# Optimization experiments

Measured on AMD Instinct MI355X. Metric: run time of the kernel, lower is better.

## Reference

```python
import jax, jax.numpy as jnp
import numpy as np

N_NODES = 50000
N_EDGES = 800000
NODE_IN = 256
EDGE_IN = 64
HEADS = 4
OUT = 64
NEG_SLOPE = 0.2  # dgl GATConv default


def setup_inputs() -> dict:
    key = jax.random.key(0)
    ks = jax.random.split(key, 10)
    node_feats = jax.random.normal(ks[0], (N_NODES, NODE_IN), dtype=jnp.float32)
    edge_feats = jax.random.normal(ks[1], (N_EDGES, EDGE_IN), dtype=jnp.float32)
    src = jax.random.randint(ks[2], (N_EDGES,), 0, N_NODES, dtype=jnp.int32)
    dst = jax.random.randint(ks[3], (N_EDGES,), 0, N_NODES, dtype=jnp.int32)
    # learned params (Xavier-ish scaling)
    W = jax.random.normal(ks[4], (NODE_IN, HEADS * OUT), dtype=jnp.float32) / np.sqrt(NODE_IN)
    We = jax.random.normal(ks[5], (EDGE_IN, HEADS * OUT), dtype=jnp.float32) / np.sqrt(EDGE_IN)
    attn_l = jax.random.normal(ks[6], (HEADS, OUT), dtype=jnp.float32) / np.sqrt(OUT)
    attn_r = jax.random.normal(ks[7], (HEADS, OUT), dtype=jnp.float32) / np.sqrt(OUT)
    attn_e = jax.random.normal(ks[8], (HEADS, OUT), dtype=jnp.float32) / np.sqrt(OUT)
    return {"node_feats": node_feats, "edge_feats": edge_feats, "W": W, "We": We,
            "attn_l": attn_l, "attn_r": attn_r, "attn_e": attn_e, "src": src, "dst": dst}


def reference(node_feats, edge_feats, W, We, attn_l, attn_r, attn_e, src, dst):
    # GAT with edge features (dropout disabled for deterministic reference).
    N = node_feats.shape[0]
    H, D = attn_l.shape
    h = (node_feats @ W).reshape(N, H, D)              # [N,H,D] projected nodes
    fe = (edge_feats @ We).reshape(-1, H, D)           # [E,H,D] projected edges
    el = jnp.sum(h * attn_l, axis=-1)                  # [N,H]
    er = jnp.sum(h * attn_r, axis=-1)                  # [N,H]
    ee = jnp.sum(fe * attn_e, axis=-1)                 # [E,H]
    e = jax.nn.leaky_relu(el[src] + er[dst] + ee, NEG_SLOPE)  # [E,H]
    # numerically stable segment softmax over incoming edges of each dst node
    emax = jax.ops.segment_max(e, dst, num_segments=N)         # [N,H]
    emax = jnp.where(jnp.isfinite(emax), emax, 0.0)            # empty segments -> 0
    ex = jnp.exp(e - emax[dst])                                # [E,H]
    denom = jax.ops.segment_sum(ex, dst, num_segments=N)       # [N,H]
    alpha = ex / (denom[dst] + 1e-9)                           # [E,H]
    out = jax.ops.segment_sum(alpha[..., None] * h[src], dst, num_segments=N)  # [N,H,D]
    return out
```

## Files before the change

### kernel.cpp

```cpp
#include <hip/hip_runtime.h>
#include <hip/hip_bf16.h>
#include <math.h>

#define N_NODES 50000
#define N_EDGES 800000
#define HEADS 4
#define HD 256
#define NEG_SLOPE 0.2f

typedef __attribute__((ext_vector_type(8))) short bf16x8;
typedef __attribute__((ext_vector_type(4))) float f32x4;

__device__ unsigned short g_Hb[N_NODES * HD];
__device__ float    g_el[N_NODES * HEADS];
__device__ float    g_er[N_NODES * HEADS];
__device__ float    g_ebuf[N_EDGES * HEADS];
__device__ float    g_esort[N_EDGES * HEADS];
__device__ int      g_srcs[N_EDGES];
__device__ int      g_deg[N_NODES];
__device__ int      g_rowptr[N_NODES + 1];
__device__ int      g_cursor[N_NODES];
__device__ int      g_bsum[256];
__device__ float    g_Wea[64 * HEADS];
__device__ unsigned short g_Wbt[256 * 256];
__device__ unsigned short g_Wlrb[16 * 256];

__device__ __forceinline__ unsigned short f2bf(float f) {
    unsigned u = __float_as_uint(f);
    u += 0x7fffu + ((u >> 16) & 1u);
    return (unsigned short)(u >> 16);
}
__device__ __forceinline__ float bf_lo(unsigned u) {
    return __uint_as_float(u << 16);
}
__device__ __forceinline__ float bf_hi(unsigned u) {
    return __uint_as_float(u & 0xFFFF0000u);
}

__global__ void k_prep2(const float* __restrict__ W, const float* __restrict__ We,
                        const float* __restrict__ al, const float* __restrict__ ar,
                        const float* __restrict__ ae) {
    int t = blockIdx.x * 256 + threadIdx.x;
    if (t < N_NODES) g_deg[t] = 0;
    if (t < 256) {
        int k = t >> 2, h = t & 3;
        float s = 0.f;
        for (int d = 0; d < 64; ++d) s += We[k * 256 + h * 64 + d] * ae[h * 64 + d];
        g_Wea[t] = s;
    }
    if (t < 4096) {
        int c = t >> 8, k = t & 255;
        float s = 0.f;
        if (c < 4) {
            for (int d = 0; d < 64; ++d) s += W[k * 256 + c * 64 + d] * al[c * 64 + d];
        } else if (c < 8) {
            int h = c - 4;
            for (int d = 0; d < 64; ++d) s += W[k * 256 + h * 64 + d] * ar[h * 64 + d];
        }
        g_Wlrb[c * 256 + k] = f2bf(s);
    }
    for (int i = t; i < 65536; i += 50176) {
        int n = i >> 8, k = i & 255;
        g_Wbt[n * 256 + k] = f2bf(W[k * 256 + n]);
    }
}

#define BM 128
#define BK 32
__global__ __launch_bounds__(256) void k_gemm_mfma(const float* __restrict__ X) {
    __shared__ unsigned short As[BM][40];
    const int tid = threadIdx.x;
    const int wave = tid >> 6, lane = tid & 63;
    const int l15 = lane & 15, lg = lane >> 4;
    const int row0 = blockIdx.x * BM;

    f32x4 acc[8][4];
    f32x4 accE[8];
    #pragma unroll
    for (int i = 0; i < 8; ++i) {
        accE[i] = (f32x4){0.f, 0.f, 0.f, 0.f};
        #pragma unroll
        for (int j = 0; j < 4; ++j) acc[i][j] = (f32x4){0.f, 0.f, 0.f, 0.f};
    }

    for (int k0 = 0; k0 < 256; k0 += BK) {
        #pragma unroll
        for (int q = 0; q < 4; ++q) {
            int f = q * 256 + tid;
            int r = f >> 3;
            int kq = (f & 7) << 2;
            int grow = row0 + r;
            float4 v = make_float4(0.f, 0.f, 0.f, 0.f);
            if (grow < N_NODES) v = *(const float4*)(X + grow * 256 + k0 + kq);
            ushort4 b;
            b.x = f2bf(v.x); b.y = f2bf(v.y); b.z = f2bf(v.z); b.w = f2bf(v.w);
            *(ushort4*)&As[r][kq] = b;
        }
        bf16x8 bfr[4];
        #pragma unroll
        for (int nf = 0; nf < 4; ++nf) {
            int n = wave * 64 + nf * 16 + l15;
            bfr[nf] = *(const bf16x8*)(g_Wbt + n * 256 + k0 + lg * 8);
        }
        bf16x8 bfrE = *(const bf16x8*)(g_Wlrb + l15 * 256 + k0 + lg * 8);
        __syncthreads();
        #pragma unroll
        for (int mf = 0; mf < 8; ++mf) {
            bf16x8 afr = *(const bf16x8*)&As[mf * 16 + l15][lg * 8];
            #pragma unroll
            for (int nf = 0; nf < 4; ++nf)
                acc[mf][nf] = __builtin_amdgcn_mfma_f32_16x16x32_bf16(
                    afr, bfr[nf], acc[mf][nf], 0, 0, 0);
            accE[mf] = __builtin_amdgcn_mfma_f32_16x16x32_bf16(
                afr, bfrE, accE[mf], 0, 0, 0);
        }
        __syncthreads();
    }
    #pragma unroll
    for (int mf = 0; mf < 8; ++mf) {
        #pragma unroll
        for (int r = 0; r < 4; ++r) {
            int grow = row0 + mf * 16 + lg * 4 + r;
            if (grow < N_NODES) {
                #pragma unroll
                for (int nf = 0; nf < 4; ++nf) {
                    int col = wave * 64 + nf * 16 + l15;
                    g_Hb[grow * 256 + col] = f2bf(acc[mf][nf][r]);
                }
                if (wave == 0) {
                    if (l15 < 4) g_el[grow * 4 + l15] = accE[mf][r];
                    else if (l15 < 8) g_er[grow * 4 + (l15 - 4)] = accE[mf][r];
                }
            }
        }
    }
}

__global__ __launch_bounds__(256) void k_edge(const float* __restrict__ EF,
                                              const int* __restrict__ src,
                                              const int* __restrict__ dst) {
    __shared__ float sEF[32][258];
    __shared__ float4 sW[64];
    const int tid = threadIdx.x;
    if (tid < 64) sW[tid] = *(const float4*)(g_Wea + tid * 4);
    const int e0 = blockIdx.x * 256;

    float p0 = 0.f, p1 = 0.f, p2 = 0.f, p3 = 0.f;
    #pragma unroll
    for (int kc = 0; kc < 2; ++kc) {
        __syncthreads();
        #pragma unroll
        for (int q = 0; q < 8; ++q) {
            int f = q * 256 + tid;
            int e = f >> 3;
            int c = (f & 7) << 2;
            float4 v = *(const float4*)(EF + (size_t)(e0 + e) * 64 + kc * 32 + c);
            sEF[c + 0][e] = v.x; sEF[c + 1][e] = v.y;
            sEF[c + 2][e] = v.z; sEF[c + 3][e] = v.w;
        }
        __syncthreads();
        #pragma unroll
        for (int k = 0; k < 32; ++k) {
            float x = sEF[k][tid];
            float4 w = sW[kc * 32 + k];
            p0 += x * w.x; p1 += x * w.y; p2 += x * w.z; p3 += x * w.w;
        }
    }
    const int eid = e0 + tid;
    const int s = src[eid], d = dst[eid];
    float4 l4 = *(const float4*)(g_el + s * 4);
    float4 r4 = *(const float4*)(g_er + d * 4);
    float e0v = p0 + l4.x + r4.x;
    float e1v = p1 + l4.y + r4.y;
    float e2v = p2 + l4.z + r4.z;
    float e3v = p3 + l4.w + r4.w;
    e0v = e0v > 0.f ? e0v : NEG_SLOPE * e0v;
    e1v = e1v > 0.f ? e1v : NEG_SLOPE * e1v;
    e2v = e2v > 0.f ? e2v : NEG_SLOPE * e2v;
    e3v = e3v > 0.f ? e3v : NEG_SLOPE * e3v;
    *(float4*)(g_ebuf + eid * 4) =
        make_float4(__expf(e0v), __expf(e1v), __expf(e2v), __expf(e3v));
    atomicAdd(&g_deg[d], 1);
}

__global__ void k_scan1() {
    __shared__ int s[256];
    int tid = threadIdx.x;
    int g = blockIdx.x * 256 + tid;
    int v = (g < N_NODES) ? g_deg[g] : 0;
    s[tid] = v; __syncthreads();
    for (int o = 1; o < 256; o <<= 1) {
        int t = (tid >= o) ? s[tid - o] : 0;
        __syncthreads();
        s[tid] += t;
        __syncthreads();
    }
    if (g < N_NODES) g_rowptr[g] = s[tid] - v;
    if (tid == 255) g_bsum[blockIdx.x] = s[255];
}

__global__ void k_scan2(int nb) {
    __shared__ int s[256];
    int tid = threadIdx.x;
    int v = (tid < nb) ? g_bsum[tid] : 0;
    s[tid] = v; __syncthreads();
    for (int o = 1; o < 256; o <<= 1) {
        int t = (tid >= o) ? s[tid - o] : 0;
        __syncthreads();
        s[tid] += t;
        __syncthreads();
    }
    if (tid < nb) g_bsum[tid] = s[tid] - v;
}

__global__ void k_scan3() {
    int g = blockIdx.x * 256 + threadIdx.x;
    if (g < N_NODES) {
        int r = g_rowptr[g] + g_bsum[blockIdx.x];
        g_rowptr[g] = r;
        g_cursor[g] = r;
    }
    if (g == 0) g_rowptr[N_NODES] = N_EDGES;
}

__global__ void k_scatter(const int* __restrict__ src, const int* __restrict__ dst) {
    int e = blockIdx.x * 256 + threadIdx.x;
    if (e < N_EDGES) {
        int p = atomicAdd(&g_cursor[dst[e]], 1);
        g_srcs[p] = src[e];
        *(float4*)(g_esort + p * 4) = *(const float4*)(g_ebuf + e * 4);
    }
}

__global__ __launch_bounds__(256) void k_agg(float* __restrict__ out) {
    int node = (blockIdx.x * 256 + threadIdx.x) >> 6;
    int lane = threadIdx.x & 63;
    if (node >= N_NODES) return;
    int start = g_rowptr[node], end = g_rowptr[node + 1];
    int myh = lane >> 4, sub = lane & 15;
    const int hoff = myh * 64 + sub * 4;

    float den = 0.f;
    float a0 = 0.f, a1 = 0.f, a2 = 0.f, a3 = 0.f;
    #pragma unroll 4
    for (int i = start; i < end; ++i) {
        float ex = g_esort[i * 4 + myh];
        int s = g_srcs[i];
        uint2 hv = *(const uint2*)(g_Hb + s * 256 + hoff);
        den += ex;
        a0 += ex * bf_lo(hv.x); a1 += ex * bf_hi(hv.x);
        a2 += ex * bf_lo(hv.y); a3 += ex * bf_hi(hv.y);
    }
    float rden = 1.0f / (den + 1e-9f);
    *(float4*)(out + node * 256 + lane * 4) =
        make_float4(a0 * rden, a1 * rden, a2 * rden, a3 * rden);
}

extern "C" void kernel_launch(void* const* d_in, const int* in_sizes, int n_in,
                              void* d_out, int out_size, void* d_ws, size_t ws_size,
                              hipStream_t stream) {
    const float* X  = (const float*)d_in[0];
    const float* EF = (const float*)d_in[1];
    const float* W  = (const float*)d_in[2];
    const float* We = (const float*)d_in[3];
    const float* al = (const float*)d_in[4];
    const float* ar = (const float*)d_in[5];
    const float* ae = (const float*)d_in[6];
    const int* src  = (const int*)d_in[7];
    const int* dst  = (const int*)d_in[8];
    float* out = (float*)d_out;

    const int nb_scan = (N_NODES + 255) / 256;

    k_prep2<<<nb_scan, 256, 0, stream>>>(W, We, al, ar, ae);
    k_gemm_mfma<<<(N_NODES + BM - 1) / BM, 256, 0, stream>>>(X);
    k_edge<<<N_EDGES / 256, 256, 0, stream>>>(EF, src, dst);
    k_scan1<<<nb_scan, 256, 0, stream>>>();
    k_scan2<<<1, 256, 0, stream>>>(nb_scan);
    k_scan3<<<nb_scan, 256, 0, stream>>>();
    k_scatter<<<(N_EDGES + 255) / 256, 256, 0, stream>>>(src, dst);
    k_agg<<<(N_NODES + 3) / 4, 256, 0, stream>>>(out);
}
```

Measured before the change: 265.6 us.

## Compute degrees upfront, scatter edge scores directly in edge kernel, single-block scan

Degree counting moves into the prep kernel, and the three-kernel scan becomes one 1024-thread block scan, so the CSR row pointers are ready before the edge kernel runs. The edge kernel then writes exp scores and source ids straight to their sorted CSR positions. This removes the separate scatter kernel and the intermediate ebuf round trip. Global buffers move to the workspace, deg is zeroed with a memset, and the aggregation unroll goes from 4 to 8. The single-block scan is serial, so it may add latency, and the atomic-ordered scatter writes from the edge kernel are uncoalesced.

```diff
diff --git a/kernel.cpp b/kernel.cpp
--- a/kernel.cpp
+++ b/kernel.cpp
@@ -11,20 +11,6 @@
 typedef __attribute__((ext_vector_type(8))) short bf16x8;
 typedef __attribute__((ext_vector_type(4))) float f32x4;
 
-__device__ unsigned short g_Hb[N_NODES * HD];
-__device__ float    g_el[N_NODES * HEADS];
-__device__ float    g_er[N_NODES * HEADS];
-__device__ float    g_ebuf[N_EDGES * HEADS];
-__device__ float    g_esort[N_EDGES * HEADS];
-__device__ int      g_srcs[N_EDGES];
-__device__ int      g_deg[N_NODES];
-__device__ int      g_rowptr[N_NODES + 1];
-__device__ int      g_cursor[N_NODES];
-__device__ int      g_bsum[256];
-__device__ float    g_Wea[64 * HEADS];
-__device__ unsigned short g_Wbt[256 * 256];
-__device__ unsigned short g_Wlrb[16 * 256];
-
 __device__ __forceinline__ unsigned short f2bf(float f) {
     unsigned u = __float_as_uint(f);
     u += 0x7fffu + ((u >> 16) & 1u);
@@ -37,16 +23,18 @@
     return __uint_as_float(u & 0xFFFF0000u);
 }
 
-__global__ void k_prep2(const float* __restrict__ W, const float* __restrict__ We,
-                        const float* __restrict__ al, const float* __restrict__ ar,
-                        const float* __restrict__ ae) {
+__global__ void k_prep(const float* __restrict__ W, const float* __restrict__ We,
+                       const float* __restrict__ al, const float* __restrict__ ar,
+                       const float* __restrict__ ae, const int* __restrict__ dst,
+                       int* __restrict__ deg, float* __restrict__ Wea,
+                       unsigned short* __restrict__ Wbt,
+                       unsigned short* __restrict__ Wlrb) {
     int t = blockIdx.x * 256 + threadIdx.x;
-    if (t < N_NODES) g_deg[t] = 0;
     if (t < 256) {
         int k = t >> 2, h = t & 3;
         float s = 0.f;
         for (int d = 0; d < 64; ++d) s += We[k * 256 + h * 64 + d] * ae[h * 64 + d];
-        g_Wea[t] = s;
+        Wea[t] = s;
     }
     if (t < 4096) {
         int c = t >> 8, k = t & 255;
@@ -57,17 +45,61 @@
             int h = c - 4;
             for (int d = 0; d < 64; ++d) s += W[k * 256 + h * 64 + d] * ar[h * 64 + d];
         }
-        g_Wlrb[c * 256 + k] = f2bf(s);
+        Wlrb[c * 256 + k] = f2bf(s);
     }
     for (int i = t; i < 65536; i += 50176) {
         int n = i >> 8, k = i & 255;
-        g_Wbt[n * 256 + k] = f2bf(W[k * 256 + n]);
-    }
+        Wbt[n * 256 + k] = f2bf(W[k * 256 + n]);
+    }
+    for (int e = t; e < N_EDGES; e += 50176)
+        atomicAdd(&deg[dst[e]], 1);
+}
+
+#define SCHUNK 49
+__global__ __launch_bounds__(1024) void k_scan(const int* __restrict__ deg,
+                                               int* __restrict__ rowptr,
+                                               int* __restrict__ cursor) {
+    __shared__ int ssum[1024];
+    const int t = threadIdx.x;
+    const int base = t * SCHUNK;
+    int loc[SCHUNK];
+    int s = 0;
+    #pragma unroll
+    for (int i = 0; i < SCHUNK; ++i) {
+        int g = base + i;
+        int v = (g < N_NODES) ? deg[g] : 0;
+        loc[i] = s;
+        s += v;
+    }
+    ssum[t] = s;
+    __syncthreads();
+    for (int o = 1; o < 1024; o <<= 1) {
+        int v = (t >= o) ? ssum[t - o] : 0;
+        __syncthreads();
+        ssum[t] += v;
+        __syncthreads();
+    }
+    int off = ssum[t] - s;
+    #pragma unroll
+    for (int i = 0; i < SCHUNK; ++i) {
+        int g = base + i;
+        if (g < N_NODES) {
+            int r = off + loc[i];
+            rowptr[g] = r;
+            cursor[g] = r;
+        }
+    }
+    if (t == 0) rowptr[N_NODES] = N_EDGES;
 }
 
 #define BM 128
 #define BK 32
-__global__ __launch_bounds__(256) void k_gemm_mfma(const float* __restrict__ X) {
+__global__ __launch_bounds__(256) void k_gemm_mfma(const float* __restrict__ X,
+                                                   const unsigned short* __restrict__ Wbt,
+                                                   const unsigned short* __restrict__ Wlrb,
+                                                   unsigned short* __restrict__ Hb,
+                                                   float* __restrict__ el,
+                                                   float* __restrict__ er) {
     __shared__ unsigned short As[BM][40];
     const int tid = threadIdx.x;
     const int wave = tid >> 6, lane = tid & 63;
@@ -100,9 +132,9 @@
         #pragma unroll
         for (int nf = 0; nf < 4; ++nf) {
             int n = wave * 64 + nf * 16 + l15;
-            bfr[nf] = *(const bf16x8*)(g_Wbt + n * 256 + k0 + lg * 8);
-        }
-        bf16x8 bfrE = *(const bf16x8*)(g_Wlrb + l15 * 256 + k0 + lg * 8);
+            bfr[nf] = *(const bf16x8*)(Wbt + n * 256 + k0 + lg * 8);
+        }
+        bf16x8 bfrE = *(const bf16x8*)(Wlrb + l15 * 256 + k0 + lg * 8);
         __syncthreads();
         #pragma unroll
         for (int mf = 0; mf < 8; ++mf) {
@@ -125,11 +157,11 @@
                 #pragma unroll
                 for (int nf = 0; nf < 4; ++nf) {
                     int col = wave * 64 + nf * 16 + l15;
-                    g_Hb[grow * 256 + col] = f2bf(acc[mf][nf][r]);
+                    Hb[grow * 256 + col] = f2bf(acc[mf][nf][r]);
                 }
                 if (wave == 0) {
-                    if (l15 < 4) g_el[grow * 4 + l15] = accE[mf][r];
-                    else if (l15 < 8) g_er[grow * 4 + (l15 - 4)] = accE[mf][r];
+                    if (l15 < 4) el[grow * 4 + l15] = accE[mf][r];
+                    else if (l15 < 8) er[grow * 4 + (l15 - 4)] = accE[mf][r];
                 }
             }
         }
@@ -138,11 +170,17 @@
 
 __global__ __launch_bounds__(256) void k_edge(const float* __restrict__ EF,
                                               const int* __restrict__ src,
-                                              const int* __restrict__ dst) {
+                                              const int* __restrict__ dst,
+                                              const float* __restrict__ el,
+                                              const float* __restrict__ er,
+                                              const float* __restrict__ Wea,
+                                              int* __restrict__ cursor,
+                                              float* __restrict__ esort,
+                                              int* __restrict__ srcs) {
     __shared__ float sEF[32][258];
     __shared__ float4 sW[64];
     const int tid = threadIdx.x;
-    if (tid < 64) sW[tid] = *(const float4*)(g_Wea + tid * 4);
+    if (tid < 64) sW[tid] = *(const float4*)(Wea + tid * 4);
     const int e0 = blockIdx.x * 256;
 
     float p0 = 0.f, p1 = 0.f, p2 = 0.f, p3 = 0.f;
@@ -168,8 +206,8 @@
     }
     const int eid = e0 + tid;
     const int s = src[eid], d = dst[eid];
-    float4 l4 = *(const float4*)(g_el + s * 4);
-    float4 r4 = *(const float4*)(g_er + d * 4);
+    float4 l4 = *(const float4*)(el + s * 4);
+    float4 r4 = *(const float4*)(er + d * 4);
     float e0v = p0 + l4.x + r4.x;
     float e1v = p1 + l4.y + r4.y;
     float e2v = p2 + l4.z + r4.z;
@@ -178,75 +216,31 @@
     e1v = e1v > 0.f ? e1v : NEG_SLOPE * e1v;
     e2v = e2v > 0.f ? e2v : NEG_SLOPE * e2v;
     e3v = e3v > 0.f ? e3v : NEG_SLOPE * e3v;
-    *(float4*)(g_ebuf + eid * 4) =
+    int p = atomicAdd(&cursor[d], 1);
+    *(float4*)(esort + (size_t)p * 4) =
         make_float4(__expf(e0v), __expf(e1v), __expf(e2v), __expf(e3v));
-    atomicAdd(&g_deg[d], 1);
-}
-
-__global__ void k_scan1() {
-    __shared__ int s[256];
-    int tid = threadIdx.x;
-    int g = blockIdx.x * 256 + tid;
-    int v = (g < N_NODES) ? g_deg[g] : 0;
-    s[tid] = v; __syncthreads();
-    for (int o = 1; o < 256; o <<= 1) {
-        int t = (tid >= o) ? s[tid - o] : 0;
-        __syncthreads();
-        s[tid] += t;
-        __syncthreads();
-    }
-    if (g < N_NODES) g_rowptr[g] = s[tid] - v;
-    if (tid == 255) g_bsum[blockIdx.x] = s[255];
-}
-
-__global__ void k_scan2(int nb) {
-    __shared__ int s[256];
-    int tid = threadIdx.x;
-    int v = (tid < nb) ? g_bsum[tid] : 0;
-    s[tid] = v; __syncthreads();
-    for (int o = 1; o < 256; o <<= 1) {
-        int t = (tid >= o) ? s[tid - o] : 0;
-        __syncthreads();
-        s[tid] += t;
-        __syncthreads();
-    }
-    if (tid < nb) g_bsum[tid] = s[tid] - v;
-}
-
-__global__ void k_scan3() {
-    int g = blockIdx.x * 256 + threadIdx.x;
-    if (g < N_NODES) {
-        int r = g_rowptr[g] + g_bsum[blockIdx.x];
-        g_rowptr[g] = r;
-        g_cursor[g] = r;
-    }
-    if (g == 0) g_rowptr[N_NODES] = N_EDGES;
-}
-
-__global__ void k_scatter(const int* __restrict__ src, const int* __restrict__ dst) {
-    int e = blockIdx.x * 256 + threadIdx.x;
-    if (e < N_EDGES) {
-        int p = atomicAdd(&g_cursor[dst[e]], 1);
-        g_srcs[p] = src[e];
-        *(float4*)(g_esort + p * 4) = *(const float4*)(g_ebuf + e * 4);
-    }
-}
-
-__global__ __launch_bounds__(256) void k_agg(float* __restrict__ out) {
+    srcs[p] = s;
+}
+
+__global__ __launch_bounds__(256) void k_agg(const int* __restrict__ rowptr,
+                                             const int* __restrict__ srcs,
+                                             const float* __restrict__ esort,
+                                             const unsigned short* __restrict__ Hb,
+                                             float* __restrict__ out) {
     int node = (blockIdx.x * 256 + threadIdx.x) >> 6;
     int lane = threadIdx.x & 63;
     if (node >= N_NODES) return;
-    int start = g_rowptr[node], end = g_rowptr[node + 1];
+    int start = rowptr[node], end = rowptr[node + 1];
     int myh = lane >> 4, sub = lane & 15;
     const int hoff = myh * 64 + sub * 4;
 
     float den = 0.f;
     float a0 = 0.f, a1 = 0.f, a2 = 0.f, a3 = 0.f;
-    #pragma unroll 4
+    #pragma unroll 8
     for (int i = start; i < end; ++i) {
-        float ex = g_esort[i * 4 + myh];
-        int s = g_srcs[i];
-        uint2 hv = *(const uint2*)(g_Hb + s * 256 + hoff);
+        float ex = esort[i * 4 + myh];
+        int s = srcs[i];
+        uint2 hv = *(const uint2*)(Hb + s * 256 + hoff);
         den += ex;
         a0 += ex * bf_lo(hv.x); a1 += ex * bf_hi(hv.x);
         a2 += ex * bf_lo(hv.y); a3 += ex * bf_hi(hv.y);
@@ -270,14 +264,30 @@
     const int* dst  = (const int*)d_in[8];
     float* out = (float*)d_out;
 
-    const int nb_scan = (N_NODES + 255) / 256;
-
-    k_prep2<<<nb_scan, 256, 0, stream>>>(W, We, al, ar, ae);
-    k_gemm_mfma<<<(N_NODES + BM - 1) / BM, 256, 0, stream>>>(X);
-    k_edge<<<N_EDGES / 256, 256, 0, stream>>>(EF, src, dst);
-    k_scan1<<<nb_scan, 256, 0, stream>>>();
-    k_scan2<<<1, 256, 0, stream>>>(nb_scan);
-    k_scan3<<<nb_scan, 256, 0, stream>>>();
-    k_scatter<<<(N_EDGES + 255) / 256, 256, 0, stream>>>(src, dst);
-    k_agg<<<(N_NODES + 3) / 4, 256, 0, stream>>>(out);
-}
+    char* ws = (char*)d_ws;
+    size_t off = 0;
+    auto alloc = [&](size_t bytes) {
+        void* p = ws + off;
+        off = (off + bytes + 255) & ~(size_t)255;
+        return p;
+    };
+    unsigned short* Hb   = (unsigned short*)alloc((size_t)N_NODES * HD * 2);
+    float*          esort= (float*)alloc((size_t)N_EDGES * 4 * 4);
+    int*            srcs = (int*)alloc((size_t)N_EDGES * 4);
+    float*          el   = (float*)alloc((size_t)N_NODES * 4 * 4);
+    float*          er   = (float*)alloc((size_t)N_NODES * 4 * 4);
+    int*            deg  = (int*)alloc((size_t)N_NODES * 4);
+    int*            rowptr=(int*)alloc((size_t)(N_NODES + 1) * 4);
+    int*            cursor=(int*)alloc((size_t)N_NODES * 4);
+    float*          Wea  = (float*)alloc(64 * HEADS * 4);
+    unsigned short* Wbt  = (unsigned short*)alloc(256 * 256 * 2);
+    unsigned short* Wlrb = (unsigned short*)alloc(16 * 256 * 2);
+    (void)ws_size;
+
+    hipMemsetAsync(deg, 0, (size_t)N_NODES * 4, stream);
+    k_prep<<<196, 256, 0, stream>>>(W, We, al, ar, ae, dst, deg, Wea, Wbt, Wlrb);
+    k_scan<<<1, 1024, 0, stream>>>(deg, rowptr, cursor);
+    k_gemm_mfma<<<(N_NODES + BM - 1) / BM, 256, 0, stream>>>(X, Wbt, Wlrb, Hb, el, er);
+    k_edge<<<N_EDGES / 256, 256, 0, stream>>>(EF, src, dst, el, er, Wea, cursor, esort, srcs);
+    k_agg<<<(N_NODES + 3) / 4, 256, 0, stream>>>(rowptr, srcs, esort, Hb, out);
+}
```

After: 328.3 us. 23.6% more time.

## Compute degrees early and scatter edge scores directly into CSR order

Applied to the files above, without the earlier changes.

Degree counting moves into the prep kernel, so the scan can run before the edge kernel. The edge kernel then writes exp scores and source ids straight to their sorted CSR slots in a packed 32-byte struct, which removes the separate scatter kernel and the intermediate edge buffer. The aggregation loop reads the packed struct and is unrolled further. The cost is an extra zeroing launch, a serial grid-stride atomic loop over the edges in prep, and padded 32-byte records that raise bytes read per edge in aggregation.

```diff
diff --git a/kernel.cpp b/kernel.cpp
--- a/kernel.cpp
+++ b/kernel.cpp
@@ -11,12 +11,16 @@
 typedef __attribute__((ext_vector_type(8))) short bf16x8;
 typedef __attribute__((ext_vector_type(4))) float f32x4;
 
+struct __align__(32) EPack {
+    float ex[4];
+    int   s;
+    int   pad[3];
+};
+
 __device__ unsigned short g_Hb[N_NODES * HD];
 __device__ float    g_el[N_NODES * HEADS];
 __device__ float    g_er[N_NODES * HEADS];
-__device__ float    g_ebuf[N_EDGES * HEADS];
-__device__ float    g_esort[N_EDGES * HEADS];
-__device__ int      g_srcs[N_EDGES];
+__device__ EPack    g_ep[N_EDGES];
 __device__ int      g_deg[N_NODES];
 __device__ int      g_rowptr[N_NODES + 1];
 __device__ int      g_cursor[N_NODES];
@@ -37,11 +41,15 @@
     return __uint_as_float(u & 0xFFFF0000u);
 }
 
-__global__ void k_prep2(const float* __restrict__ W, const float* __restrict__ We,
-                        const float* __restrict__ al, const float* __restrict__ ar,
-                        const float* __restrict__ ae) {
+__global__ void k_zero() {
+    int g = blockIdx.x * 256 + threadIdx.x;
+    if (g < N_NODES) g_deg[g] = 0;
+}
+
+__global__ void k_prep(const float* __restrict__ W, const float* __restrict__ We,
+                       const float* __restrict__ al, const float* __restrict__ ar,
+                       const float* __restrict__ ae, const int* __restrict__ dst) {
     int t = blockIdx.x * 256 + threadIdx.x;
-    if (t < N_NODES) g_deg[t] = 0;
     if (t < 256) {
         int k = t >> 2, h = t & 3;
         float s = 0.f;
@@ -63,6 +71,8 @@
         int n = i >> 8, k = i & 255;
         g_Wbt[n * 256 + k] = f2bf(W[k * 256 + n]);
     }
+    for (int e = t; e < N_EDGES; e += 50176)
+        atomicAdd(&g_deg[dst[e]], 1);
 }
 
 #define BM 128
@@ -136,6 +146,46 @@
     }
 }
 
+__global__ void k_scan1() {
+    __shared__ int s[256];
+    int tid = threadIdx.x;
+    int g = blockIdx.x * 256 + tid;
+    int v = (g < N_NODES) ? g_deg[g] : 0;
+    s[tid] = v; __syncthreads();
+    for (int o = 1; o < 256; o <<= 1) {
+        int t = (tid >= o) ? s[tid - o] : 0;
+        __syncthreads();
+        s[tid] += t;
+        __syncthreads();
+    }
+    if (g < N_NODES) g_rowptr[g] = s[tid] - v;
+    if (tid == 255) g_bsum[blockIdx.x] = s[255];
+}
+
+__global__ void k_scan2(int nb) {
+    __shared__ int s[256];
+    int tid = threadIdx.x;
+    int v = (tid < nb) ? g_bsum[tid] : 0;
+    s[tid] = v; __syncthreads();
+    for (int o = 1; o < 256; o <<= 1) {
+        int t = (tid >= o) ? s[tid - o] : 0;
+        __syncthreads();
+        s[tid] += t;
+        __syncthreads();
+    }
+    if (tid < nb) g_bsum[tid] = s[tid] - v;
+}
+
+__global__ void k_scan3() {
+    int g = blockIdx.x * 256 + threadIdx.x;
+    if (g < N_NODES) {
+        int r = g_rowptr[g] + g_bsum[blockIdx.x];
+        g_rowptr[g] = r;
+        g_cursor[g] = r;
+    }
+    if (g == 0) g_rowptr[N_NODES] = N_EDGES;
+}
+
 __global__ __launch_bounds__(256) void k_edge(const float* __restrict__ EF,
                                               const int* __restrict__ src,
                                               const int* __restrict__ dst) {
@@ -178,58 +228,10 @@
     e1v = e1v > 0.f ? e1v : NEG_SLOPE * e1v;
     e2v = e2v > 0.f ? e2v : NEG_SLOPE * e2v;
     e3v = e3v > 0.f ? e3v : NEG_SLOPE * e3v;
-    *(float4*)(g_ebuf + eid * 4) =
+    int p = atomicAdd(&g_cursor[d], 1);
+    *(float4*)g_ep[p].ex =
         make_float4(__expf(e0v), __expf(e1v), __expf(e2v), __expf(e3v));
-    atomicAdd(&g_deg[d], 1);
-}
-
-__global__ void k_scan1() {
-    __shared__ int s[256];
-    int tid = threadIdx.x;
-    int g = blockIdx.x * 256 + tid;
-    int v = (g < N_NODES) ? g_deg[g] : 0;
-    s[tid] = v; __syncthreads();
-    for (int o = 1; o < 256; o <<= 1) {
-        int t = (tid >= o) ? s[tid - o] : 0;
-        __syncthreads();
-        s[tid] += t;
-        __syncthreads();
-    }
-    if (g < N_NODES) g_rowptr[g] = s[tid] - v;
-    if (tid == 255) g_bsum[blockIdx.x] = s[255];
-}
-
-__global__ void k_scan2(int nb) {
-    __shared__ int s[256];
-    int tid = threadIdx.x;
-    int v = (tid < nb) ? g_bsum[tid] : 0;
-    s[tid] = v; __syncthreads();
-    for (int o = 1; o < 256; o <<= 1) {
-        int t = (tid >= o) ? s[tid - o] : 0;
-        __syncthreads();
-        s[tid] += t;
-        __syncthreads();
-    }
-    if (tid < nb) g_bsum[tid] = s[tid] - v;
-}
-
-__global__ void k_scan3() {
-    int g = blockIdx.x * 256 + threadIdx.x;
-    if (g < N_NODES) {
-        int r = g_rowptr[g] + g_bsum[blockIdx.x];
-        g_rowptr[g] = r;
-        g_cursor[g] = r;
-    }
-    if (g == 0) g_rowptr[N_NODES] = N_EDGES;
-}
-
-__global__ void k_scatter(const int* __restrict__ src, const int* __restrict__ dst) {
-    int e = blockIdx.x * 256 + threadIdx.x;
-    if (e < N_EDGES) {
-        int p = atomicAdd(&g_cursor[dst[e]], 1);
-        g_srcs[p] = src[e];
-        *(float4*)(g_esort + p * 4) = *(const float4*)(g_ebuf + e * 4);
-    }
+    g_ep[p].s = s;
 }
 
 __global__ __launch_bounds__(256) void k_agg(float* __restrict__ out) {
@@ -242,10 +244,10 @@
 
     float den = 0.f;
     float a0 = 0.f, a1 = 0.f, a2 = 0.f, a3 = 0.f;
-    #pragma unroll 4
+    #pragma unroll 8
     for (int i = start; i < end; ++i) {
-        float ex = g_esort[i * 4 + myh];
-        int s = g_srcs[i];
+        float ex = g_ep[i].ex[myh];
+        int s = g_ep[i].s;
         uint2 hv = *(const uint2*)(g_Hb + s * 256 + hoff);
         den += ex;
         a0 += ex * bf_lo(hv.x); a1 += ex * bf_hi(hv.x);
@@ -272,12 +274,12 @@
 
     const int nb_scan = (N_NODES + 255) / 256;
 
-    k_prep2<<<nb_scan, 256, 0, stream>>>(W, We, al, ar, ae);
+    k_zero<<<nb_scan, 256, 0, stream>>>();
+    k_prep<<<nb_scan, 256, 0, stream>>>(W, We, al, ar, ae, dst);
     k_gemm_mfma<<<(N_NODES + BM - 1) / BM, 256, 0, stream>>>(X);
-    k_edge<<<N_EDGES / 256, 256, 0, stream>>>(EF, src, dst);
     k_scan1<<<nb_scan, 256, 0, stream>>>();
     k_scan2<<<1, 256, 0, stream>>>(nb_scan);
     k_scan3<<<nb_scan, 256, 0, stream>>>();
-    k_scatter<<<(N_EDGES + 255) / 256, 256, 0, stream>>>(src, dst);
+    k_edge<<<N_EDGES / 256, 256, 0, stream>>>(EF, src, dst);
     k_agg<<<(N_NODES + 3) / 4, 256, 0, stream>>>(out);
 }
```

Measured after the change: 257.3 us. 3.1% less time.
